# Kernel tuning notes

Hardware: AMD Instinct MI355X
Metric: run time of the kernel (lower is better)

Reference implementation:

```python
import jax, jax.numpy as jnp
import numpy as np
jax.config.update("jax_enable_x64", True)

N = 16384   # nodes
C = 16      # initial color vocabulary size
B = 64      # number of graphs in the batch
_rs = np.random.RandomState(42)
_MULTS = jnp.asarray((_rs.randint(1, 2 ** 62, size=C + 1).astype(np.int64) << 1) | 1)  # odd 64-bit hash multipliers


def setup_inputs() -> dict:
    key = jax.random.key(0)
    k1, k2, k3 = jax.random.split(key, 3)
    x = jax.random.randint(k1, (N,), 0, C, dtype=jnp.int64)
    adj_t = jax.random.randint(k2, (N, N), 0, 2).astype(jnp.float32)  # dense binary adjacency
    batch = jnp.sort(jax.random.randint(k3, (N,), 0, B, dtype=jnp.int64))
    return {"x": x, "adj_t": adj_t, "batch": batch}


def _wl_colors(x, adj_t):
    # One WL refinement step. The torch code hashes (own_color, sorted neighbor colors)
    # and assigns new ids by insertion order into an OrderedDict ('isolate' -> 0).
    # A sorted tuple of neighbor colors is equivalent to the neighbor color multiset,
    # which we represent as a count histogram and hash with a 64-bit wraparound
    # polynomial hash; ids are then assigned by first-occurrence (node-index) order.
    n = x.shape[0]
    onehot = jax.nn.one_hot(x, C, dtype=adj_t.dtype)                 # [N, C]
    nbr_hist = jnp.round(adj_t @ onehot).astype(jnp.int64)           # [N, C] neighbor color counts
    iso = (adj_t.sum(axis=1) + adj_t.sum(axis=0)) == 0               # isolated nodes
    h = x * _MULTS[0] + (nbr_hist * _MULTS[1:]).sum(axis=-1)         # int64 wraparound hash
    h = jnp.where(iso, jnp.int64(-(2 ** 63)), h)
    order = jnp.argsort(h)
    hs = h[order]
    new_grp = jnp.concatenate([jnp.ones((1,), bool), hs[1:] != hs[:-1]])
    gid = jnp.zeros(n, jnp.int64).at[order].set(jnp.cumsum(new_grp) - 1)   # group id per node
    first_of_grp = jax.ops.segment_min(jnp.arange(n), gid, num_segments=n)
    firsts = first_of_grp[gid]                                       # first node index with same signature
    is_first = (~iso) & (firsts == jnp.arange(n))
    rank = jnp.cumsum(is_first.astype(jnp.int64))                    # hashmap insertion order (1-based)
    return jnp.where(iso, 0, rank[firsts])                           # 'isolate' -> 0


def _histogram(colors, batch):
    # Per-graph color histogram; width padded to N+1 (max possible distinct colors)
    # for static shapes -- extra columns are zero and do not affect the L2 norm.
    num_colors = N + 1
    idx = batch * num_colors + colors
    out = jnp.zeros(B * num_colors, jnp.int64).at[idx].add(1)
    out = out.reshape(B, num_colors)[:, 1:]                          # drop 'isolate' column
    out = out.astype(jnp.float64)
    return out / jnp.linalg.norm(out, axis=-1, keepdims=True)


def reference(x, adj_t, batch):
    colors = _wl_colors(x, adj_t)          # forward's default return value
    hist = _histogram(colors, batch)       # return_embedding=True output
    return hist, colors
```

## Files before the change

### kernel.cpp

```cpp
#include <hip/hip_runtime.h>
#include <stdint.h>

#define NN 16384
#define NC 16
#define NB 64

struct Mults { unsigned long long m[17]; };


__global__ __launch_bounds__(256) void k_table(const int* __restrict__ x,
                                               unsigned long long* __restrict__ table,
                                               int* __restrict__ scount) {
  if (blockIdx.x == 0 && threadIdx.x == 0) *scount = 0;
  int idx = blockIdx.x * 256 + threadIdx.x;
  int c = idx & 15, k = (idx >> 4) & 3, chunk = idx >> 6;
  unsigned long long m = 0ull;
  for (int l = 0; l < 64; ++l) {
    int col = chunk * 256 + l * 4 + k;
    if (x[col] == c) m |= (1ull << l);
  }
  table[idx] = m;
}

__global__ __launch_bounds__(256) void k_hist(const float* __restrict__ adj,
                                              const unsigned long long* __restrict__ table,
                                              const int* __restrict__ x,
                                              Mults M,
                                              unsigned long long* __restrict__ h,
                                              int* __restrict__ iso,
                                              int* __restrict__ firsts,
                                              int* __restrict__ suspects,
                                              int* __restrict__ scount) {
  int wave = threadIdx.x >> 6;
  int lane = threadIdx.x & 63;
  int row  = blockIdx.x * 4 + wave;
  int xv   = x[row];
  const uint4* rowp = (const uint4*)(adj + (size_t)row * NN);
  int c = lane & 15, k = lane >> 4;
  const unsigned long long* tk = table + (k * 16 + c);
  int cnt = 0;
  for (int chunk = 0; chunk < 64; ++chunk) {
    uint4 v = rowp[chunk * 64 + lane];
    unsigned long long b0 = __ballot(v.x != 0u);
    unsigned long long b1 = __ballot(v.y != 0u);
    unsigned long long b2 = __ballot(v.z != 0u);
    unsigned long long b3 = __ballot(v.w != 0u);
    unsigned long long m = (k & 2) ? ((k & 1) ? b3 : b2) : ((k & 1) ? b1 : b0);
    cnt += __popcll(m & tk[chunk * 64]);
  }
  cnt += __shfl_xor(cnt, 16, 64);
  cnt += __shfl_xor(cnt, 32, 64);
  int rs = cnt;
  rs += __shfl_xor(rs, 1, 64);
  rs += __shfl_xor(rs, 2, 64);
  rs += __shfl_xor(rs, 4, 64);
  rs += __shfl_xor(rs, 8, 64);
  unsigned long long hl = (unsigned long long)(long long)cnt * M.m[(lane & 15) + 1];
  hl += __shfl_xor(hl, 1, 64);
  hl += __shfl_xor(hl, 2, 64);
  hl += __shfl_xor(hl, 4, 64);
  hl += __shfl_xor(hl, 8, 64);
  if (lane == 0) {
    h[row] = hl + (unsigned long long)(long long)xv * M.m[0];
    if (rs == 0) { int s = atomicAdd(scount, 1); suspects[s] = row; }
  }
  if (lane == 1) iso[row] = 0;
  if (lane == 2) firsts[row] = 0x7fffffff;
}

__global__ __launch_bounds__(256) void k_colcheck(const float* __restrict__ adj,
                                                  const int* __restrict__ suspects,
                                                  const int* __restrict__ scount,
                                                  int* __restrict__ iso,
                                                  unsigned long long* __restrict__ h) {
  __shared__ int red[256];
  int nsus = *scount;
  for (int u = blockIdx.x; u < nsus; u += gridDim.x) {
    int col = suspects[u];
    int any = 0;
    for (int r = threadIdx.x; r < NN; r += 256)
      any |= (adj[(size_t)r * NN + col] != 0.0f);
    red[threadIdx.x] = any;
    __syncthreads();
    for (int s = 128; s > 0; s >>= 1) {
      if (threadIdx.x < s) red[threadIdx.x] |= red[threadIdx.x + s];
      __syncthreads();
    }
    if (threadIdx.x == 0 && red[0] == 0) {
      iso[col] = 1;
      h[col] = 0x8000000000000000ull;
    }
    __syncthreads();
  }
}

#define JC 2048
__global__ __launch_bounds__(256) void k_firsts(const unsigned long long* __restrict__ h,
                                                int* __restrict__ firsts) {
  __shared__ unsigned long long hs[JC];
  int jbase = blockIdx.y * JC;
  for (int t = threadIdx.x; t < JC; t += 256) hs[t] = h[jbase + t];
  __syncthreads();
  int i = blockIdx.x * 256 + threadIdx.x;
  unsigned long long hi = h[i];
  int best = 0x7fffffff;
  for (int jj = 0; jj < JC; ++jj) {
    if (hs[jj] == hi) best = min(best, jbase + jj);
  }
  if (best < 0x7fffffff) atomicMin(&firsts[i], best);
}

__global__ __launch_bounds__(1024) void k_scan(const int* __restrict__ iso,
                                               const int* __restrict__ firsts,
                                               const int* __restrict__ batch,
                                               float* __restrict__ out_colors,
                                               int* __restrict__ cnt) {
  __shared__ int rank_lds[NN];
  __shared__ int sums[1024];
  int t = threadIdx.x;
  int base = t * 16;
  int loc[16];
  int s = 0;
  for (int u = 0; u < 16; ++u) {
    int i = base + u;
    int isf = (!iso[i]) && (firsts[i] == i);
    s += isf;
    loc[u] = s;
  }
  sums[t] = s;
  __syncthreads();
  for (int off = 1; off < 1024; off <<= 1) {
    int add = (t >= off) ? sums[t - off] : 0;
    __syncthreads();
    sums[t] += add;
    __syncthreads();
  }
  int excl = sums[t] - s;
  for (int u = 0; u < 16; ++u) rank_lds[base + u] = excl + loc[u];
  __syncthreads();
  for (int u = 0; u < 16; ++u) {
    int i = base + u;
    int c = iso[i] ? 0 : rank_lds[firsts[i]];
    out_colors[i] = (float)c;
    if (c > 0) atomicAdd(&cnt[(size_t)batch[i] * NN + (c - 1)], 1);
  }
}

__global__ __launch_bounds__(256) void k_norm(const int* __restrict__ cnt,
                                              float* __restrict__ out) {
  __shared__ float red[256];
  int b = blockIdx.x;
  float ss = 0.0f;
  for (int j = threadIdx.x; j < NN; j += 256) {
    float v = (float)cnt[(size_t)b * NN + j];
    ss += v * v;
  }
  red[threadIdx.x] = ss;
  __syncthreads();
  for (int s = 128; s > 0; s >>= 1) {
    if (threadIdx.x < s) red[threadIdx.x] += red[threadIdx.x + s];
    __syncthreads();
  }
  float nrm = sqrtf(red[0]);
  for (int j = threadIdx.x; j < NN; j += 256)
    out[(size_t)b * NN + j] = (float)cnt[(size_t)b * NN + j] / nrm;
}


struct MTState { uint32_t mt[624]; int idx; };

static void mt_seed(MTState& s, uint32_t seed) {
  s.mt[0] = seed;
  for (int i = 1; i < 624; ++i)
    s.mt[i] = 1812433253u * (s.mt[i - 1] ^ (s.mt[i - 1] >> 30)) + (uint32_t)i;
  s.idx = 624;
}

static uint32_t mt_next(MTState& s) {
  if (s.idx >= 624) {
    for (int i = 0; i < 624; ++i) {
      uint32_t y = (s.mt[i] & 0x80000000u) | (s.mt[(i + 1) % 624] & 0x7fffffffu);
      uint32_t nx = s.mt[(i + 397) % 624] ^ (y >> 1);
      if (y & 1u) nx ^= 2567483615u;
      s.mt[i] = nx;
    }
    s.idx = 0;
  }
  uint32_t y = s.mt[s.idx++];
  y ^= y >> 11;
  y ^= (y << 7) & 2636928640u;
  y ^= (y << 15) & 4022730752u;
  y ^= y >> 18;
  return y;
}

static uint64_t mt_next64(MTState& s) {
  uint64_t hi = mt_next(s);
  uint64_t lo = mt_next(s);
  return (hi << 32) | lo;
}


extern "C" void kernel_launch(void* const* d_in, const int* in_sizes, int n_in,
                              void* d_out, int out_size, void* d_ws, size_t ws_size,
                              hipStream_t stream) {
  const int*   x     = (const int*)d_in[0];
  const float* adj   = (const float*)d_in[1];
  const int*   batch = (const int*)d_in[2];
  float* out_hist   = (float*)d_out;
  float* out_colors = out_hist + (size_t)NB * NN;

  char* ws = (char*)d_ws;
  int*                cnt      = (int*)(ws + 0);
  int*                scount   = (int*)(ws + 4194304);
  int*                suspects = (int*)(ws + 4194560);
  unsigned long long* h        = (unsigned long long*)(ws + 4260096);
  int*                iso      = (int*)(ws + 4391168);
  int*                firsts   = (int*)(ws + 4456704);
  unsigned long long* table    = (unsigned long long*)(ws + 4522240);

  Mults M;
  {
    MTState st;
    mt_seed(st, 42u);
    const uint64_t mask62 = (1ull << 62) - 1ull;
    const uint64_t rng    = (1ull << 62) - 2ull;
    for (int i = 0; i < 17; ++i) {
      uint64_t v;
      do { v = mt_next64(st) & mask62; } while (v > rng);
      M.m[i] = ((1ull + v) << 1) | 1ull;
    }
  }

  hipMemsetAsync(cnt, 0, (size_t)NB * NN * 4, stream);
  k_table<<<16, 256, 0, stream>>>(x, table, scount);
  k_hist<<<NN / 4, 256, 0, stream>>>(adj, table, x, M, h, iso, firsts, suspects, scount);
  k_colcheck<<<64, 256, 0, stream>>>(adj, suspects, scount, iso, h);
  dim3 gf(NN / 256, NN / JC);
  k_firsts<<<gf, 256, 0, stream>>>(h, firsts);
  k_scan<<<1, 1024, 0, stream>>>(iso, firsts, batch, out_colors, cnt);
  k_norm<<<NB, 256, 0, stream>>>(cnt, out_hist);
}
```

Before: 1.469 ms.

## Fuse memset into init, vectorize loads, use wave-shuffle scan and unrolls

```diff
diff --git a/kernel.cpp b/kernel.cpp
--- a/kernel.cpp
+++ b/kernel.cpp
@@ -5,21 +5,30 @@
 #define NC 16
 #define NB 64
 
+typedef unsigned int vuint4 __attribute__((ext_vector_type(4)));
+
 struct Mults { unsigned long long m[17]; };
 
 
-__global__ __launch_bounds__(256) void k_table(const int* __restrict__ x,
-                                               unsigned long long* __restrict__ table,
-                                               int* __restrict__ scount) {
-  if (blockIdx.x == 0 && threadIdx.x == 0) *scount = 0;
+__global__ __launch_bounds__(256) void k_init(const int* __restrict__ x,
+                                              unsigned long long* __restrict__ table,
+                                              int* __restrict__ scount,
+                                              int* __restrict__ cnt) {
   int idx = blockIdx.x * 256 + threadIdx.x;
-  int c = idx & 15, k = (idx >> 4) & 3, chunk = idx >> 6;
-  unsigned long long m = 0ull;
-  for (int l = 0; l < 64; ++l) {
-    int col = chunk * 256 + l * 4 + k;
-    if (x[col] == c) m |= (1ull << l);
-  }
-  table[idx] = m;
+  if (idx == 0) *scount = 0;
+  if (idx < 4096) {
+    int c = idx & 15, k = (idx >> 4) & 3, chunk = idx >> 6;
+    unsigned long long m = 0ull;
+    for (int l = 0; l < 64; ++l) {
+      int col = chunk * 256 + l * 4 + k;
+      if (x[col] == c) m |= (1ull << l);
+    }
+    table[idx] = m;
+  }
+  int4 z = {0, 0, 0, 0};
+  int4* c4 = (int4*)cnt;
+  #pragma unroll
+  for (int r = 0; r < 4; ++r) c4[(size_t)idx * 4 + r] = z;
 }
 
 __global__ __launch_bounds__(256) void k_hist(const float* __restrict__ adj,
@@ -35,18 +44,21 @@
   int lane = threadIdx.x & 63;
   int row  = blockIdx.x * 4 + wave;
   int xv   = x[row];
-  const uint4* rowp = (const uint4*)(adj + (size_t)row * NN);
-  int c = lane & 15, k = lane >> 4;
+  const vuint4* rowp = (const vuint4*)(adj + (size_t)row * NN);
+  int c = lane & 15, k = lane >> 6 ? 0 : (lane >> 4);
+  k = lane >> 4;
   const unsigned long long* tk = table + (k * 16 + c);
   int cnt = 0;
+  #pragma unroll 4
   for (int chunk = 0; chunk < 64; ++chunk) {
-    uint4 v = rowp[chunk * 64 + lane];
+    vuint4 v = __builtin_nontemporal_load(&rowp[chunk * 64 + lane]);
+    unsigned long long tm = tk[chunk * 64];
     unsigned long long b0 = __ballot(v.x != 0u);
     unsigned long long b1 = __ballot(v.y != 0u);
     unsigned long long b2 = __ballot(v.z != 0u);
     unsigned long long b3 = __ballot(v.w != 0u);
     unsigned long long m = (k & 2) ? ((k & 1) ? b3 : b2) : ((k & 1) ? b1 : b0);
-    cnt += __popcll(m & tk[chunk * 64]);
+    cnt += __popcll(m & tm);
   }
   cnt += __shfl_xor(cnt, 16, 64);
   cnt += __shfl_xor(cnt, 32, 64);
@@ -104,6 +116,7 @@
   int i = blockIdx.x * 256 + threadIdx.x;
   unsigned long long hi = h[i];
   int best = 0x7fffffff;
+  #pragma unroll 8
   for (int jj = 0; jj < JC; ++jj) {
     if (hs[jj] == hi) best = min(best, jbase + jj);
   }
@@ -116,28 +129,38 @@
                                                float* __restrict__ out_colors,
                                                int* __restrict__ cnt) {
   __shared__ int rank_lds[NN];
-  __shared__ int sums[1024];
+  __shared__ int wsum[16];
   int t = threadIdx.x;
+  int lane = t & 63, wv = t >> 6;
   int base = t * 16;
   int loc[16];
   int s = 0;
+  #pragma unroll
   for (int u = 0; u < 16; ++u) {
     int i = base + u;
     int isf = (!iso[i]) && (firsts[i] == i);
     s += isf;
     loc[u] = s;
   }
-  sums[t] = s;
-  __syncthreads();
-  for (int off = 1; off < 1024; off <<= 1) {
-    int add = (t >= off) ? sums[t - off] : 0;
-    __syncthreads();
-    sums[t] += add;
-    __syncthreads();
-  }
-  int excl = sums[t] - s;
+  int incl = s;
+  #pragma unroll
+  for (int off = 1; off < 64; off <<= 1) {
+    int v = __shfl_up(incl, off, 64);
+    if (lane >= off) incl += v;
+  }
+  if (lane == 63) wsum[wv] = incl;
+  __syncthreads();
+  if (t == 0) {
+    int acc = 0;
+    #pragma unroll
+    for (int w = 0; w < 16; ++w) { int v = wsum[w]; wsum[w] = acc; acc += v; }
+  }
+  __syncthreads();
+  int excl = wsum[wv] + incl - s;
+  #pragma unroll
   for (int u = 0; u < 16; ++u) rank_lds[base + u] = excl + loc[u];
   __syncthreads();
+  #pragma unroll
   for (int u = 0; u < 16; ++u) {
     int i = base + u;
     int c = iso[i] ? 0 : rank_lds[firsts[i]];
@@ -150,10 +173,13 @@
                                               float* __restrict__ out) {
   __shared__ float red[256];
   int b = blockIdx.x;
+  const int4* c4 = (const int4*)(cnt + (size_t)b * NN);
+  float4* o4 = (float4*)(out + (size_t)b * NN);
   float ss = 0.0f;
-  for (int j = threadIdx.x; j < NN; j += 256) {
-    float v = (float)cnt[(size_t)b * NN + j];
-    ss += v * v;
+  for (int j = threadIdx.x; j < NN / 4; j += 256) {
+    int4 v = c4[j];
+    float4 f = {(float)v.x, (float)v.y, (float)v.z, (float)v.w};
+    ss += f.x * f.x + f.y * f.y + f.z * f.z + f.w * f.w;
   }
   red[threadIdx.x] = ss;
   __syncthreads();
@@ -161,9 +187,12 @@
     if (threadIdx.x < s) red[threadIdx.x] += red[threadIdx.x + s];
     __syncthreads();
   }
-  float nrm = sqrtf(red[0]);
-  for (int j = threadIdx.x; j < NN; j += 256)
-    out[(size_t)b * NN + j] = (float)cnt[(size_t)b * NN + j] / nrm;
+  float inv = 1.0f / sqrtf(red[0]);
+  for (int j = threadIdx.x; j < NN / 4; j += 256) {
+    int4 v = c4[j];
+    float4 f = {(float)v.x * inv, (float)v.y * inv, (float)v.z * inv, (float)v.w * inv};
+    o4[j] = f;
+  }
 }
 
 
@@ -232,8 +261,7 @@
     }
   }
 
-  hipMemsetAsync(cnt, 0, (size_t)NB * NN * 4, stream);
-  k_table<<<16, 256, 0, stream>>>(x, table, scount);
+  k_init<<<256, 256, 0, stream>>>(x, table, scount, cnt);
   k_hist<<<NN / 4, 256, 0, stream>>>(adj, table, x, M, h, iso, firsts, suspects, scount);
   k_colcheck<<<64, 256, 0, stream>>>(adj, suspects, scount, iso, h);
   dim3 gf(NN / 256, NN / JC);
```

After: 1.402 ms. 4.6% less time.
